# Kernel optimization log

Hardware: AMD Instinct MI355X
Metric: run time of the kernel (lower is better)

Reference implementation:

```python
import jax, jax.numpy as jnp
import numpy as np

N = 50000      # nodes
E = 400000     # edges
CIN = 15
HID = 128
HEADS = 4
NC = 2
EPS_BN = 1e-5


def _bn(x, g, b, m, v):
    # BatchNorm1d in eval mode: running stats
    return g * (x - m) * jax.lax.rsqrt(v + EPS_BN) + b


def _gat(x, src, dst, w, a_s, a_d, bias):
    # PyG GATConv(heads=4, concat=False): adds self-loops, per-head attention,
    # softmax over incoming edges (grouped by dst), mean over heads + bias.
    sl = jnp.arange(N, dtype=src.dtype)
    src = jnp.concatenate([src, sl]); dst = jnp.concatenate([dst, sl])
    h = (x @ w).reshape(N, HEADS, HID)                     # [N,H,C]
    a_src = jnp.einsum('nhc,hc->nh', h, a_s)               # [N,H]
    a_dst = jnp.einsum('nhc,hc->nh', h, a_d)
    e = jax.nn.leaky_relu(a_src[src] + a_dst[dst], 0.2)    # [E',H]
    m = jax.ops.segment_max(e, dst, num_segments=N)        # stable segment softmax
    ex = jnp.exp(e - m[dst])
    s = jax.ops.segment_sum(ex, dst, num_segments=N)
    alpha = ex / (s[dst] + 1e-16)
    out = jax.ops.segment_sum(alpha[:, :, None] * h[src], dst, num_segments=N)
    return out.mean(axis=1) + bias                         # concat=False -> head mean


def _gcn(x, src, dst, ew, w, bias):
    # PyG GCNConv with edge_weight: self-loops (weight 1), symmetric normalization.
    sl = jnp.arange(N, dtype=src.dtype)
    src_f = jnp.concatenate([src, sl]); dst_f = jnp.concatenate([dst, sl])
    ew_f = jnp.concatenate([ew, jnp.ones((N,), ew.dtype)])
    deg = jax.ops.segment_sum(ew_f, dst_f, num_segments=N)
    dinv = jnp.where(deg > 0, jax.lax.rsqrt(jnp.maximum(deg, 1e-12)), 0.0)
    norm = dinv[src_f] * ew_f * dinv[dst_f]
    h = x @ w
    return jax.ops.segment_sum(norm[:, None] * h[src_f], dst_f, num_segments=N) + bias


def setup_inputs() -> dict:
    key = jax.random.key(0)
    ks = iter(jax.random.split(key, 40))
    nrm = lambda s, sc: jax.random.normal(next(ks), s, jnp.float32) * sc
    H2 = HID // 2
    inp = {
        'x': jax.random.normal(next(ks), (N, CIN), jnp.float32),
        'edge_index': jax.random.randint(next(ks), (2, E), 0, N, jnp.int32),
        'edge_attr': jax.random.uniform(next(ks), (E, 1), jnp.float32),
        # GATConv params
        'w_gat': nrm((CIN, HEADS * HID), 0.25),
        'att_src': nrm((HEADS, HID), 0.1),
        'att_dst': nrm((HEADS, HID), 0.1),
        'b_gat': jnp.zeros((HID,), jnp.float32),
        # GCNConv params
        'w2': nrm((HID, HID), 0.09), 'b2': jnp.zeros((HID,), jnp.float32),
        'w3': nrm((HID, HID), 0.09), 'b3': jnp.zeros((HID,), jnp.float32),
        'w4': nrm((HID, HID), 0.09), 'b4': jnp.zeros((HID,), jnp.float32),
        # BatchNorm (4 layers stacked): gamma, beta, running_mean, running_var
        'bn_g': 1.0 + nrm((4, HID), 0.1),
        'bn_b': nrm((4, HID), 0.1),
        'bn_m': nrm((4, HID), 0.1),
        'bn_v': 1.0 + 0.1 * jax.random.uniform(next(ks), (4, HID), jnp.float32),
        # dense heads
        'w_shared': nrm((HID, HID), 0.09), 'b_shared': jnp.zeros((HID,), jnp.float32),
        'w_mask1': nrm((HID, H2), 0.09), 'b_mask1': jnp.zeros((H2,), jnp.float32),
        'w_mask2': nrm((H2, NC), 0.12), 'b_mask2': jnp.zeros((NC,), jnp.float32),
        'w_inst1': nrm((HID, H2), 0.09), 'b_inst1': jnp.zeros((H2,), jnp.float32),
        'w_inst2': nrm((H2, NC), 0.12), 'b_inst2': jnp.zeros((NC,), jnp.float32),
        'w_edge1': nrm((HID, H2), 0.09), 'b_edge1': jnp.zeros((H2,), jnp.float32),
        'w_edge2': nrm((H2, 1), 0.12), 'b_edge2': jnp.zeros((1,), jnp.float32),
    }
    return inp


def reference(x, edge_index, edge_attr, w_gat, att_src, att_dst, b_gat,
              w2, b2, w3, b3, w4, b4, bn_g, bn_b, bn_m, bn_v,
              w_shared, b_shared, w_mask1, b_mask1, w_mask2, b_mask2,
              w_inst1, b_inst1, w_inst2, b_inst2, w_edge1, b_edge1, w_edge2, b_edge2):
    src, dst = edge_index[0], edge_index[1]
    ew = edge_attr.squeeze(-1)
    h = jax.nn.relu(_bn(_gat(x, src, dst, w_gat, att_src, att_dst, b_gat),
                        bn_g[0], bn_b[0], bn_m[0], bn_v[0]))
    h = jax.nn.relu(_bn(_gcn(h, src, dst, ew, w2, b2), bn_g[1], bn_b[1], bn_m[1], bn_v[1]))
    h = jax.nn.relu(_bn(_gcn(h, src, dst, ew, w3, b3), bn_g[2], bn_b[2], bn_m[2], bn_v[2]))
    h = jax.nn.relu(_bn(_gcn(h, src, dst, ew, w4, b4), bn_g[3], bn_b[3], bn_m[3], bn_v[3]))
    hs = jax.nn.relu(h @ w_shared + b_shared)
    hm = jax.nn.relu(hs @ w_mask1 + b_mask1)
    mask_out = hm @ w_mask2 + b_mask2
    hi = jax.nn.relu(hs @ w_inst1 + b_inst1)
    instance_out = hi @ w_inst2 + b_inst2
    he = jax.nn.relu(hs @ w_edge1 + b_edge1)
    edge_out = he @ w_edge2 + b_edge2
    return (mask_out, instance_out, edge_out)
```

## Files before the change

kernel.cpp:

```cpp
#include <hip/hip_runtime.h>
#include <hip/hip_bf16.h>

#define NNODES 50000
#define NEDGES 400000
#define ETOT   (NEDGES + NNODES)
#define CIN    15
#define HID    128
#define HEADS  4
#define EPS_BN 1e-5f
#define NB_SCAN ((NNODES + 255) / 256)
#define NTILES  ((NNODES + 63) / 64)

typedef __attribute__((ext_vector_type(8))) short bf16x8_t;
typedef __attribute__((ext_vector_type(4))) float f32x4_t;

__device__ __forceinline__ float bfu(unsigned short u) {
  return __uint_as_float(((unsigned)u) << 16);
}
__device__ __forceinline__ unsigned short f2bf(float x) {
  union { __hip_bfloat16 b; unsigned short u; } c;
  c.b = __float2bfloat16(x);
  return c.u;
}
__device__ __forceinline__ float lrelu02(float x) {
  return x > 0.0f ? x : 0.2f * x;
}

template <int WPT, int KT, int NBLK>
__global__ __launch_bounds__(256) void gemm_mfma_kernel(
    const float* __restrict__ A, const unsigned short* __restrict__ WTh,
    const unsigned short* __restrict__ WTl, const float* __restrict__ bias,
    const float* __restrict__ bg, const float* __restrict__ bb,
    const float* __restrict__ bm, const float* __restrict__ bv,
    void* __restrict__ Cout, int act, int obf16) {
  constexpr int NC = WPT * 64;
  constexpr int CST = NC + 4;
  constexpr int CPR = KT / 8;
  constexpr int NKC = KT / 32;
  constexpr int ABYTES = 64 * KT * 2 * 2;
  constexpr int CBYTES = 64 * CST * 4;
  constexpr int SBYTES = (ABYTES > CBYTES) ? ABYTES : CBYTES;
  __shared__ __align__(16) char smem[SBYTES];
  unsigned short* Ah = (unsigned short*)smem;
  unsigned short* Al = Ah + 64 * KT;
  float* Cs = (float*)smem;

  const int tid = threadIdx.x;
  const int wv = tid >> 6, l = tid & 63;
  const int lcol = l & 15;
  const int kg = (l >> 4) << 3;
  const int colbase = wv * (WPT * 16);

  bf16x8_t hbh[NKC][WPT], hbl[NKC][WPT];
#pragma unroll
  for (int kc = 0; kc < NKC; ++kc)
#pragma unroll
    for (int jj = 0; jj < WPT; ++jj) {
      size_t boff = (size_t)(colbase + jj * 16 + lcol) * KT + kc * 32 + kg;
      hbh[kc][jj] = *(const bf16x8_t*)(WTh + boff);
      hbl[kc][jj] = *(const bf16x8_t*)(WTl + boff);
    }

  for (int tile = blockIdx.x; tile < NTILES; tile += NBLK) {
    const int bm_ = tile * 64;
    __syncthreads();

#pragma unroll
    for (int i = 0; i < (64 * CPR) / 256; ++i) {
      int cch = tid + 256 * i;
      int r = cch / CPR, k0 = (cch % CPR) << 3;
      int gr = bm_ + r;
      float v[8];
      if (gr < NNODES) {
        float4 v0 = *(const float4*)&A[(size_t)gr * KT + k0];
        float4 v1 = *(const float4*)&A[(size_t)gr * KT + k0 + 4];
        v[0] = v0.x; v[1] = v0.y; v[2] = v0.z; v[3] = v0.w;
        v[4] = v1.x; v[5] = v1.y; v[6] = v1.z; v[7] = v1.w;
      } else {
#pragma unroll
        for (int j = 0; j < 8; ++j) v[j] = 0.0f;
      }
      bf16x8_t hv, lv;
#pragma unroll
      for (int j = 0; j < 8; ++j) {
        unsigned short h = f2bf(v[j]);
        hv[j] = (short)h;
        lv[j] = (short)f2bf(v[j] - bfu(h));
      }
      int byte = (k0 << 1) ^ ((r & 7) << 4);
      *(bf16x8_t*)((char*)(Ah + r * KT) + byte) = hv;
      *(bf16x8_t*)((char*)(Al + r * KT) + byte) = lv;
    }
    __syncthreads();

    f32x4_t acc[4][WPT];
#pragma unroll
    for (int rt = 0; rt < 4; ++rt)
#pragma unroll
      for (int jj = 0; jj < WPT; ++jj) acc[rt][jj] = (f32x4_t){0.f, 0.f, 0.f, 0.f};

#pragma unroll
    for (int kc = 0; kc < NKC; ++kc) {
      int k = kc * 32 + kg;
#pragma unroll
      for (int rt = 0; rt < 4; ++rt) {
        int lrow = rt * 16 + (l & 15);
        int byte = (k << 1) ^ ((lrow & 7) << 4);
        bf16x8_t ah = *(const bf16x8_t*)((const char*)(Ah + lrow * KT) + byte);
        bf16x8_t al = *(const bf16x8_t*)((const char*)(Al + lrow * KT) + byte);
#pragma unroll
        for (int jj = 0; jj < WPT; ++jj) {
          acc[rt][jj] = __builtin_amdgcn_mfma_f32_16x16x32_bf16(ah, hbh[kc][jj], acc[rt][jj], 0, 0, 0);
          acc[rt][jj] = __builtin_amdgcn_mfma_f32_16x16x32_bf16(ah, hbl[kc][jj], acc[rt][jj], 0, 0, 0);
          acc[rt][jj] = __builtin_amdgcn_mfma_f32_16x16x32_bf16(al, hbh[kc][jj], acc[rt][jj], 0, 0, 0);
        }
      }
    }

    __syncthreads();
#pragma unroll
    for (int rt = 0; rt < 4; ++rt) {
      int trow0 = rt * 16 + ((l >> 4) << 2);
#pragma unroll
      for (int jj = 0; jj < WPT; ++jj) {
        int col = colbase + jj * 16 + lcol;
        float bs = bias ? bias[col] : 0.0f;
#pragma unroll
        for (int r = 0; r < 4; ++r) {
          float vv = acc[rt][jj][r] + bs;
          if (bg) vv = bg[col] * (vv - bm[col]) * rsqrtf(bv[col] + EPS_BN) + bb[col];
          if (act) vv = fmaxf(vv, 0.0f);
          Cs[(trow0 + r) * CST + col] = vv;
        }
      }
    }
    __syncthreads();

    constexpr int NJ = (64 * NC) / 1024;
#pragma unroll
    for (int j = 0; j < NJ; ++j) {
      int f = tid * 4 + j * 1024;
      int r = f / NC, c = f - r * NC;
      int grow = bm_ + r;
      if (grow >= NNODES) continue;
      float4 v = *(const float4*)&Cs[r * CST + c];
      if (obf16) {
        ushort4 us;
        us.x = f2bf(v.x); us.y = f2bf(v.y); us.z = f2bf(v.z); us.w = f2bf(v.w);
        *(ushort4*)&((unsigned short*)Cout)[(size_t)grow * NC + c] = us;
      } else {
        *(float4*)&((float*)Cout)[(size_t)grow * NC + c] = v;
      }
    }
  }
}

template <int NBLK>
__global__ __launch_bounds__(256) void shared_heads_kernel(
    const float* __restrict__ A, const unsigned short* __restrict__ WSh,
    const unsigned short* __restrict__ WSl, const float* __restrict__ b_shared,
    const unsigned short* __restrict__ W2h, const unsigned short* __restrict__ W2l,
    const float* __restrict__ b192,
    const float* __restrict__ w_m2, const float* __restrict__ b_m2,
    const float* __restrict__ w_i2, const float* __restrict__ b_i2,
    const float* __restrict__ w_e2, const float* __restrict__ b_e2,
    float* __restrict__ out) {
  constexpr int KT = 128;
  constexpr int CST = 196;
  constexpr int AC_BYTES = 64 * CST * 4;
  __shared__ __align__(16) char smem[AC_BYTES + 64 * KT * 2 * 2];
  unsigned short* Ah = (unsigned short*)smem;
  unsigned short* Al = Ah + 64 * KT;
  float* Cs = (float*)smem;
  unsigned short* Hh = (unsigned short*)(smem + AC_BYTES);
  unsigned short* Hl = Hh + 64 * KT;

  const int tid = threadIdx.x;
  const int wv = tid >> 6, l = tid & 63;
  const int lcol = l & 15;
  const int kg = (l >> 4) << 3;

  bf16x8_t sbh[4][2], sbl[4][2];
  {
    const int colbase = wv * 32;
#pragma unroll
    for (int kc = 0; kc < 4; ++kc)
#pragma unroll
      for (int jj = 0; jj < 2; ++jj) {
        size_t boff = (size_t)(colbase + jj * 16 + lcol) * KT + kc * 32 + kg;
        sbh[kc][jj] = *(const bf16x8_t*)(WSh + boff);
        sbl[kc][jj] = *(const bf16x8_t*)(WSl + boff);
      }
  }

  for (int tile = blockIdx.x; tile < NTILES; tile += NBLK) {
    const int bm_ = tile * 64;
    __syncthreads();

#pragma unroll
    for (int i = 0; i < 4; ++i) {
      int cch = tid + 256 * i;
      int r = cch >> 4, k0 = (cch & 15) << 3;
      int gr = bm_ + r;
      float v[8];
      if (gr < NNODES) {
        float4 v0 = *(const float4*)&A[(size_t)gr * KT + k0];
        float4 v1 = *(const float4*)&A[(size_t)gr * KT + k0 + 4];
        v[0] = v0.x; v[1] = v0.y; v[2] = v0.z; v[3] = v0.w;
        v[4] = v1.x; v[5] = v1.y; v[6] = v1.z; v[7] = v1.w;
      } else {
#pragma unroll
        for (int j = 0; j < 8; ++j) v[j] = 0.0f;
      }
      bf16x8_t hv, lv;
#pragma unroll
      for (int j = 0; j < 8; ++j) {
        unsigned short h = f2bf(v[j]);
        hv[j] = (short)h;
        lv[j] = (short)f2bf(v[j] - bfu(h));
      }
      int byte = (k0 << 1) ^ ((r & 7) << 4);
      *(bf16x8_t*)((char*)(Ah + r * KT) + byte) = hv;
      *(bf16x8_t*)((char*)(Al + r * KT) + byte) = lv;
    }
    __syncthreads();

    {
      const int colbase = wv * 32;
      f32x4_t acc[4][2];
#pragma unroll
      for (int rt = 0; rt < 4; ++rt)
#pragma unroll
        for (int jj = 0; jj < 2; ++jj) acc[rt][jj] = (f32x4_t){0.f, 0.f, 0.f, 0.f};
#pragma unroll
      for (int kc = 0; kc < 4; ++kc) {
        int k = kc * 32 + kg;
#pragma unroll
        for (int rt = 0; rt < 4; ++rt) {
          int lrow = rt * 16 + (l & 15);
          int byte = (k << 1) ^ ((lrow & 7) << 4);
          bf16x8_t ah = *(const bf16x8_t*)((const char*)(Ah + lrow * KT) + byte);
          bf16x8_t al = *(const bf16x8_t*)((const char*)(Al + lrow * KT) + byte);
#pragma unroll
          for (int jj = 0; jj < 2; ++jj) {
            acc[rt][jj] = __builtin_amdgcn_mfma_f32_16x16x32_bf16(ah, sbh[kc][jj], acc[rt][jj], 0, 0, 0);
            acc[rt][jj] = __builtin_amdgcn_mfma_f32_16x16x32_bf16(ah, sbl[kc][jj], acc[rt][jj], 0, 0, 0);
            acc[rt][jj] = __builtin_amdgcn_mfma_f32_16x16x32_bf16(al, sbh[kc][jj], acc[rt][jj], 0, 0, 0);
          }
        }
      }
#pragma unroll
      for (int rt = 0; rt < 4; ++rt) {
        int trow0 = rt * 16 + ((l >> 4) << 2);
#pragma unroll
        for (int jj = 0; jj < 2; ++jj) {
          int col = colbase + jj * 16 + lcol;
          float bs = b_shared[col];
#pragma unroll
          for (int r = 0; r < 4; ++r) {
            int trow = trow0 + r;
            float vv = fmaxf(acc[rt][jj][r] + bs, 0.0f);
            unsigned short hv = f2bf(vv);
            unsigned short lv = f2bf(vv - bfu(hv));
            int byte = ((trow * KT + col) << 1) ^ ((trow & 7) << 4);
            *(unsigned short*)((char*)Hh + byte) = hv;
            *(unsigned short*)((char*)Hl + byte) = lv;
          }
        }
      }
    }
    __syncthreads();

    {
      const int colbase = wv * 48;
      f32x4_t acc[4][3];
#pragma unroll
      for (int rt = 0; rt < 4; ++rt)
#pragma unroll
        for (int jj = 0; jj < 3; ++jj) acc[rt][jj] = (f32x4_t){0.f, 0.f, 0.f, 0.f};
#pragma unroll
      for (int kc = 0; kc < 4; ++kc) {
        bf16x8_t cbh[3], cbl[3];
#pragma unroll
        for (int jj = 0; jj < 3; ++jj) {
          size_t boff = (size_t)(colbase + jj * 16 + lcol) * KT + kc * 32 + kg;
          cbh[jj] = *(const bf16x8_t*)(W2h + boff);
          cbl[jj] = *(const bf16x8_t*)(W2l + boff);
        }
        int k = kc * 32 + kg;
#pragma unroll
        for (int rt = 0; rt < 4; ++rt) {
          int lrow = rt * 16 + (l & 15);
          int byte = (k << 1) ^ ((lrow & 7) << 4);
          bf16x8_t ah = *(const bf16x8_t*)((const char*)(Hh + lrow * KT) + byte);
          bf16x8_t al = *(const bf16x8_t*)((const char*)(Hl + lrow * KT) + byte);
#pragma unroll
          for (int jj = 0; jj < 3; ++jj) {
            acc[rt][jj] = __builtin_amdgcn_mfma_f32_16x16x32_bf16(ah, cbh[jj], acc[rt][jj], 0, 0, 0);
            acc[rt][jj] = __builtin_amdgcn_mfma_f32_16x16x32_bf16(ah, cbl[jj], acc[rt][jj], 0, 0, 0);
            acc[rt][jj] = __builtin_amdgcn_mfma_f32_16x16x32_bf16(al, cbh[jj], acc[rt][jj], 0, 0, 0);
          }
        }
      }
#pragma unroll
      for (int rt = 0; rt < 4; ++rt) {
        int trow0 = rt * 16 + ((l >> 4) << 2);
#pragma unroll
        for (int jj = 0; jj < 3; ++jj) {
          int col = colbase + jj * 16 + lcol;
          float bs = b192[col];
#pragma unroll
          for (int r = 0; r < 4; ++r) {
            float vv = fmaxf(acc[rt][jj][r] + bs, 0.0f);
            Cs[(trow0 + r) * CST + col] = vv;
          }
        }
      }
    }
    __syncthreads();

    {
      int r = tid >> 2, q = tid & 3;
      int grow = bm_ + r;
      const float* row = &Cs[r * CST];
      float p0 = 0.f, p1 = 0.f, p2 = 0.f, p3 = 0.f, p4 = 0.f;
#pragma unroll
      for (int e = 0; e < 16; ++e) {
        int c = q * 16 + e;
        float hm = row[c], hi = row[64 + c], he = row[128 + c];
        p0 += hm * w_m2[c * 2 + 0];
        p1 += hm * w_m2[c * 2 + 1];
        p2 += hi * w_i2[c * 2 + 0];
        p3 += hi * w_i2[c * 2 + 1];
        p4 += he * w_e2[c];
      }
#pragma unroll
      for (int off = 1; off < 4; off <<= 1) {
        p0 += __shfl_xor(p0, off);
        p1 += __shfl_xor(p1, off);
        p2 += __shfl_xor(p2, off);
        p3 += __shfl_xor(p3, off);
        p4 += __shfl_xor(p4, off);
      }
      if (q == 0 && grow < NNODES) {
        out[grow * 2 + 0] = p0 + b_m2[0];
        out[grow * 2 + 1] = p1 + b_m2[1];
        out[2 * NNODES + grow * 2 + 0] = p2 + b_i2[0];
        out[2 * NNODES + grow * 2 + 1] = p3 + b_i2[1];
        out[4 * NNODES + grow] = p4 + b_e2[0];
      }
    }
  }
}

__global__ void prep_att_kernel(const float* __restrict__ w,
                                const float* __restrict__ att_s,
                                const float* __restrict__ att_d,
                                float* __restrict__ wv_s,
                                float* __restrict__ wv_d) {
  int t = threadIdx.x;
  if (t >= 60) return;
  int k = t / 4, h = t & 3;
  float s = 0.f, d = 0.f;
  for (int c = 0; c < 128; ++c) {
    float wk = w[(size_t)k * 512 + h * 128 + c];
    s += wk * att_s[h * 128 + c];
    d += wk * att_d[h * 128 + c];
  }
  wv_s[k * 4 + h] = s;
  wv_d[k * 4 + h] = d;
}

__global__ void pack_wtp_kernel(const float* __restrict__ w,
                                unsigned short* __restrict__ WTh,
                                unsigned short* __restrict__ WTl) {
  int i = blockIdx.x * blockDim.x + threadIdx.x;
  if (i >= 128 * 64) return;
  int c = i >> 6, j = i & 63;
  float xv = 0.f;
  if (j < 60) {
    int h = j / 15, k = j - h * 15;
    xv = 0.25f * w[(size_t)k * 512 + h * 128 + c];
  }
  unsigned short hh = f2bf(xv);
  WTh[i] = hh;
  WTl[i] = f2bf(xv - bfu(hh));
}

__global__ __launch_bounds__(256) void a_sd_kernel(
    const float* __restrict__ x, const float* __restrict__ wv_s,
    const float* __restrict__ wv_d, float* __restrict__ a_s,
    float* __restrict__ a_d) {
  __shared__ float xs[256 * 15];
  __shared__ float wvs[60], wvd[60];
  int t = threadIdx.x;
  int base = blockIdx.x * 256;
  if (t < 60) { wvs[t] = wv_s[t]; wvd[t] = wv_d[t]; }
  for (int i = t; i < 256 * 15; i += 256) {
    int gi = base * 15 + i;
    xs[i] = (gi < NNODES * 15) ? x[gi] : 0.0f;
  }
  __syncthreads();
  int n = base + t;
  if (n >= NNODES) return;
  float a0 = 0, a1 = 0, a2 = 0, a3 = 0, d0 = 0, d1 = 0, d2 = 0, d3 = 0;
#pragma unroll
  for (int k = 0; k < 15; ++k) {
    float xv = xs[t * 15 + k];
    a0 += xv * wvs[k * 4 + 0]; a1 += xv * wvs[k * 4 + 1];
    a2 += xv * wvs[k * 4 + 2]; a3 += xv * wvs[k * 4 + 3];
    d0 += xv * wvd[k * 4 + 0]; d1 += xv * wvd[k * 4 + 1];
    d2 += xv * wvd[k * 4 + 2]; d3 += xv * wvd[k * 4 + 3];
  }
  float4 A; A.x = a0; A.y = a1; A.z = a2; A.w = a3;
  float4 D; D.x = d0; D.y = d1; D.z = d2; D.w = d3;
  *(float4*)&a_s[n * 4] = A;
  *(float4*)&a_d[n * 4] = D;
}

__global__ __launch_bounds__(256) void gat_fused_kernel(
    const float* __restrict__ x, const float* __restrict__ a_s,
    const float* __restrict__ a_d, const int* __restrict__ rowptr,
    const int* __restrict__ csr_src, float* __restrict__ g) {
  int wid = threadIdx.x >> 6, lane = threadIdx.x & 63;
  int n = blockIdx.x * 4 + wid;
  if (n >= NNODES) return;
  int e0 = rowptr[n], e1 = rowptr[n + 1];
  bool on = lane < 60;
  int h = on ? (lane / 15) : 0;
  int k = on ? (lane - h * 15) : 0;
  float adn = a_d[n * 4 + h];

  float ssum = 0.f, acc = 0.f;
  int e = e0;
  for (; e + 4 <= e1; e += 4) {
    int s0 = csr_src[e + 0], s1 = csr_src[e + 1];
    int s2 = csr_src[e + 2], s3 = csr_src[e + 3];
    float as0 = a_s[s0 * 4 + h], as1 = a_s[s1 * 4 + h];
    float as2 = a_s[s2 * 4 + h], as3 = a_s[s3 * 4 + h];
    float x0 = x[(size_t)s0 * CIN + k], x1 = x[(size_t)s1 * CIN + k];
    float x2 = x[(size_t)s2 * CIN + k], x3 = x[(size_t)s3 * CIN + k];
    float ex0 = __expf(lrelu02(as0 + adn));
    float ex1 = __expf(lrelu02(as1 + adn));
    float ex2 = __expf(lrelu02(as2 + adn));
    float ex3 = __expf(lrelu02(as3 + adn));
    ssum += (ex0 + ex1) + (ex2 + ex3);
    acc += ex0 * x0 + ex1 * x1 + ex2 * x2 + ex3 * x3;
  }
  for (; e < e1; ++e) {
    int s = csr_src[e];
    float ex = __expf(lrelu02(a_s[s * 4 + h] + adn));
    ssum += ex;
    acc += ex * x[(size_t)s * CIN + k];
  }
  g[(size_t)n * 64 + lane] = on ? acc / (ssum + 1e-16f) : 0.0f;
}

__global__ void pack_wt4_kernel(
    const float* __restrict__ w2, const float* __restrict__ w3,
    const float* __restrict__ w4, const float* __restrict__ ws,
    unsigned short* __restrict__ Hbase, unsigned short* __restrict__ Lbase) {
  int i = blockIdx.x * blockDim.x + threadIdx.x;
  if (i >= 128 * 128) return;
  const float* W = (blockIdx.y == 0) ? w2 : (blockIdx.y == 1) ? w3
                 : (blockIdx.y == 2) ? w4 : ws;
  unsigned short* Wh = Hbase + (size_t)blockIdx.y * 128 * 128;
  unsigned short* Wl = Lbase + (size_t)blockIdx.y * 128 * 128;
  int k = i >> 7, n = i & 127;
  float x = W[i];
  unsigned short h = f2bf(x);
  Wh[n * 128 + k] = h;
  Wl[n * 128 + k] = f2bf(x - bfu(h));
}

__global__ void pack_wt192_kernel(
    const float* __restrict__ w_m1, const float* __restrict__ w_i1,
    const float* __restrict__ w_e1, const float* __restrict__ b_m1,
    const float* __restrict__ b_i1, const float* __restrict__ b_e1,
    unsigned short* __restrict__ WTh, unsigned short* __restrict__ WTl,
    float* __restrict__ b192) {
  int i = blockIdx.x * blockDim.x + threadIdx.x;
  if (i < 192 * 128) {
    int n = i >> 7, k = i & 127;
    float x = (n < 64) ? w_m1[k * 64 + n]
            : (n < 128) ? w_i1[k * 64 + (n - 64)]
                        : w_e1[k * 64 + (n - 128)];
    unsigned short h = f2bf(x);
    WTh[(size_t)n * 128 + k] = h;
    WTl[(size_t)n * 128 + k] = f2bf(x - bfu(h));
  }
  if (i < 192) {
    b192[i] = (i < 64) ? b_m1[i] : (i < 128) ? b_i1[i - 64] : b_e1[i - 128];
  }
}

__global__ void count_deg_kernel(const int* __restrict__ ei,
                                 const float* __restrict__ ea,
                                 int* __restrict__ cnt,
                                 float* __restrict__ deg) {
  int i = blockIdx.x * blockDim.x + threadIdx.x;
  if (i >= ETOT) return;
  int d; float w;
  if (i < NEDGES) { d = ei[NEDGES + i]; w = ea[i]; }
  else            { d = i - NEDGES; w = 1.0f; }
  atomicAdd(&cnt[d], 1);
  atomicAdd(&deg[d], w);
}

__global__ __launch_bounds__(256) void csr_reduce_kernel(
    const int* __restrict__ cnt, int* __restrict__ bsum) {
  __shared__ int red[256];
  int t = threadIdx.x;
  int i = blockIdx.x * 256 + t;
  red[t] = (i < NNODES) ? cnt[i] : 0;
  __syncthreads();
  for (int off = 128; off > 0; off >>= 1) {
    if (t < off) red[t] += red[t + off];
    __syncthreads();
  }
  if (t == 0) bsum[blockIdx.x] = red[0];
}

__global__ __launch_bounds__(256) void csr_scanb_kernel(
    const int* __restrict__ bsum, int* __restrict__ boff) {
  __shared__ int s[256];
  int t = threadIdx.x;
  s[t] = (t < NB_SCAN) ? bsum[t] : 0;
  __syncthreads();
  for (int off = 1; off < 256; off <<= 1) {
    int u = (t >= off) ? s[t - off] : 0;
    __syncthreads();
    s[t] += u;
    __syncthreads();
  }
  if (t < NB_SCAN) boff[t] = (t == 0) ? 0 : s[t - 1];
}

__global__ __launch_bounds__(256) void csr_scan_kernel(
    int* __restrict__ cnt, const int* __restrict__ boff,
    int* __restrict__ rowptr) {
  __shared__ int s[256];
  int t = threadIdx.x;
  int i = blockIdx.x * 256 + t;
  int v = (i < NNODES) ? cnt[i] : 0;
  s[t] = v;
  __syncthreads();
  for (int off = 1; off < 256; off <<= 1) {
    int u = (t >= off) ? s[t - off] : 0;
    __syncthreads();
    s[t] += u;
    __syncthreads();
  }
  if (i < NNODES) {
    rowptr[i] = boff[blockIdx.x] + s[t] - v;
    cnt[i] = 0;
  }
  if (i == 0) rowptr[NNODES] = ETOT;
}

__global__ void dinv_kernel(const float* __restrict__ deg,
                            float* __restrict__ dinv) {
  int n = blockIdx.x * blockDim.x + threadIdx.x;
  if (n >= NNODES) return;
  float s = deg[n];
  dinv[n] = (s > 0.0f) ? rsqrtf(fmaxf(s, 1e-12f)) : 0.0f;
}

__global__ void scatter_kernel(const int* __restrict__ ei,
                               const float* __restrict__ ea,
                               const float* __restrict__ dinv,
                               const int* __restrict__ rowptr,
                               int* __restrict__ cursor,
                               int* __restrict__ csr_src,
                               float* __restrict__ csr_ew) {
  int i = blockIdx.x * blockDim.x + threadIdx.x;
  if (i >= ETOT) return;
  int s, d; float w;
  if (i < NEDGES) { s = ei[i]; d = ei[NEDGES + i]; w = ea[i]; }
  else            { s = d = i - NEDGES; w = 1.0f; }
  int pos = rowptr[d] + atomicAdd(&cursor[d], 1);
  csr_src[pos] = s;
  csr_ew[pos] = dinv[s] * w * dinv[d];
}

__global__ __launch_bounds__(256) void gcn_gather_kernel(
    const __hip_bfloat16* __restrict__ h, const int* __restrict__ rowptr,
    const int* __restrict__ csr_src, const float* __restrict__ csr_w,
    const float* __restrict__ bias,
    const float* __restrict__ bg, const float* __restrict__ bb,
    const float* __restrict__ bm, const float* __restrict__ bv,
    float* __restrict__ out) {
  int wid = threadIdx.x >> 6, lane = threadIdx.x & 63;
  int n = blockIdx.x * 4 + wid;
  if (n >= NNODES) return;
  int e0 = rowptr[n], e1 = rowptr[n + 1];
  int c = 2 * lane;
  float ax = 0.f, ay = 0.f;
  int e = e0;
  for (; e + 4 <= e1; e += 4) {
    int s0 = csr_src[e + 0], s1 = csr_src[e + 1];
    int s2 = csr_src[e + 2], s3 = csr_src[e + 3];
    float w0 = csr_w[e + 0], w1 = csr_w[e + 1];
    float w2 = csr_w[e + 2], w3 = csr_w[e + 3];
    ushort2 u0 = *(const ushort2*)(h + (size_t)s0 * HID + c);
    ushort2 u1 = *(const ushort2*)(h + (size_t)s1 * HID + c);
    ushort2 u2 = *(const ushort2*)(h + (size_t)s2 * HID + c);
    ushort2 u3 = *(const ushort2*)(h + (size_t)s3 * HID + c);
    ax += w0 * bfu(u0.x) + w1 * bfu(u1.x) + w2 * bfu(u2.x) + w3 * bfu(u3.x);
    ay += w0 * bfu(u0.y) + w1 * bfu(u1.y) + w2 * bfu(u2.y) + w3 * bfu(u3.y);
  }
  for (; e < e1; ++e) {
    int s = csr_src[e];
    float w = csr_w[e];
    ushort2 u = *(const ushort2*)(h + (size_t)s * HID + c);
    ax += w * bfu(u.x);
    ay += w * bfu(u.y);
  }
  float ox = ax + bias[c];
  float oy = ay + bias[c + 1];
  ox = bg[c] * (ox - bm[c]) * rsqrtf(bv[c] + EPS_BN) + bb[c];
  oy = bg[c + 1] * (oy - bm[c + 1]) * rsqrtf(bv[c + 1] + EPS_BN) + bb[c + 1];
  ox = fmaxf(ox, 0.0f); oy = fmaxf(oy, 0.0f);
  float2 o; o.x = ox; o.y = oy;
  *(float2*)&out[(size_t)n * HID + c] = o;
}

extern "C" void kernel_launch(void* const* d_in, const int* in_sizes, int n_in,
                              void* d_out, int out_size, void* d_ws, size_t ws_size,
                              hipStream_t stream) {
  const float* x       = (const float*)d_in[0];
  const int*   ei      = (const int*)d_in[1];
  const float* ea      = (const float*)d_in[2];
  const float* w_gat   = (const float*)d_in[3];
  const float* att_src = (const float*)d_in[4];
  const float* att_dst = (const float*)d_in[5];
  const float* b_gat   = (const float*)d_in[6];
  const float* w2 = (const float*)d_in[7];  const float* b2 = (const float*)d_in[8];
  const float* w3 = (const float*)d_in[9];  const float* b3 = (const float*)d_in[10];
  const float* w4 = (const float*)d_in[11]; const float* b4 = (const float*)d_in[12];
  const float* bn_g = (const float*)d_in[13];
  const float* bn_b = (const float*)d_in[14];
  const float* bn_m = (const float*)d_in[15];
  const float* bn_v = (const float*)d_in[16];
  const float* w_shared = (const float*)d_in[17]; const float* b_shared = (const float*)d_in[18];
  const float* w_m1 = (const float*)d_in[19]; const float* b_m1 = (const float*)d_in[20];
  const float* w_m2 = (const float*)d_in[21]; const float* b_m2 = (const float*)d_in[22];
  const float* w_i1 = (const float*)d_in[23]; const float* b_i1 = (const float*)d_in[24];
  const float* w_i2 = (const float*)d_in[25]; const float* b_i2 = (const float*)d_in[26];
  const float* w_e1 = (const float*)d_in[27]; const float* b_e1 = (const float*)d_in[28];
  const float* w_e2 = (const float*)d_in[29]; const float* b_e2 = (const float*)d_in[30];
  float* out = (float*)d_out;

  size_t off = 0;
  auto alloc = [&](size_t bytes) -> char* {
    char* p = (char*)d_ws + off;
    off += (bytes + 255) & ~(size_t)255;
    return p;
  };
  float* p0      = (float*)alloc((size_t)NNODES * HID * 4);
  float* p1      = (float*)alloc((size_t)NNODES * HID * 4);
  float* g       = (float*)alloc((size_t)NNODES * 64 * 4);
  __hip_bfloat16* hb = (__hip_bfloat16*)alloc((size_t)NNODES * HID * 2);
  float* a_s     = (float*)alloc((size_t)NNODES * 4 * 4);
  float* a_d     = (float*)alloc((size_t)NNODES * 4 * 4);
  float* deg     = (float*)alloc((size_t)NNODES * 4);
  float* dinv    = (float*)alloc((size_t)NNODES * 4);
  float* csr_ew  = (float*)alloc((size_t)ETOT * 4);
  int*   rowptr  = (int*)alloc((size_t)(NNODES + 1) * 4);
  int*   cnt     = (int*)alloc((size_t)NNODES * 4);
  int*   csr_src = (int*)alloc((size_t)ETOT * 4);
  int*   bsum    = (int*)alloc((size_t)NB_SCAN * 4);
  int*   boff    = (int*)alloc((size_t)NB_SCAN * 4);
  unsigned short* wtH = (unsigned short*)alloc(4 * 128 * 128 * 2);
  unsigned short* wtL = (unsigned short*)alloc(4 * 128 * 128 * 2);
  unsigned short* wt192h = (unsigned short*)alloc(192 * 128 * 2);
  unsigned short* wt192l = (unsigned short*)alloc(192 * 128 * 2);
  unsigned short* wtph = (unsigned short*)alloc(128 * 64 * 2);
  unsigned short* wtpl = (unsigned short*)alloc(128 * 64 * 2);
  float* b192 = (float*)alloc(192 * 4);
  float* wv_s = (float*)alloc(60 * 4);
  float* wv_d = (float*)alloc(60 * 4);

  unsigned short* wt2h = wtH + 0 * 16384; unsigned short* wt2l = wtL + 0 * 16384;
  unsigned short* wt3h = wtH + 1 * 16384; unsigned short* wt3l = wtL + 1 * 16384;
  unsigned short* wt4h = wtH + 2 * 16384; unsigned short* wt4l = wtL + 2 * 16384;
  unsigned short* wsh  = wtH + 3 * 16384; unsigned short* wsl  = wtL + 3 * 16384;

  dim3 blk256(256);
  dim3 wgrid((NNODES + 3) / 4);

  hipMemsetAsync(cnt, 0, NNODES * 4, stream);
  hipMemsetAsync(deg, 0, NNODES * 4, stream);
  count_deg_kernel<<<(ETOT + 255) / 256, blk256, 0, stream>>>(ei, ea, cnt, deg);
  csr_reduce_kernel<<<NB_SCAN, blk256, 0, stream>>>(cnt, bsum);
  csr_scanb_kernel<<<1, blk256, 0, stream>>>(bsum, boff);
  csr_scan_kernel<<<NB_SCAN, blk256, 0, stream>>>(cnt, boff, rowptr);
  dinv_kernel<<<(NNODES + 255) / 256, blk256, 0, stream>>>(deg, dinv);
  scatter_kernel<<<(ETOT + 255) / 256, blk256, 0, stream>>>(
      ei, ea, dinv, rowptr, cnt, csr_src, csr_ew);

  prep_att_kernel<<<1, 64, 0, stream>>>(w_gat, att_src, att_dst, wv_s, wv_d);
  pack_wtp_kernel<<<(128 * 64 + 255) / 256, blk256, 0, stream>>>(w_gat, wtph, wtpl);
  pack_wt4_kernel<<<dim3((128 * 128 + 255) / 256, 4), blk256, 0, stream>>>(
      w2, w3, w4, w_shared, wtH, wtL);
  pack_wt192_kernel<<<(192 * 128 + 255) / 256, blk256, 0, stream>>>(
      w_m1, w_i1, w_e1, b_m1, b_i1, b_e1, wt192h, wt192l, b192);

  a_sd_kernel<<<NB_SCAN, blk256, 0, stream>>>(x, wv_s, wv_d, a_s, a_d);

  gat_fused_kernel<<<wgrid, blk256, 0, stream>>>(
      x, a_s, a_d, rowptr, csr_src, g);

  gemm_mfma_kernel<2, 64, 512><<<512, blk256, 0, stream>>>(
      g, wtph, wtpl, b_gat, bn_g + 0, bn_b + 0, bn_m + 0, bn_v + 0, p0, 1, 0);

  gemm_mfma_kernel<2, 128, 512><<<512, blk256, 0, stream>>>(
      p0, wt2h, wt2l, nullptr, nullptr, nullptr, nullptr, nullptr, hb, 0, 1);
  gcn_gather_kernel<<<wgrid, blk256, 0, stream>>>(
      hb, rowptr, csr_src, csr_ew, b2,
      bn_g + 128, bn_b + 128, bn_m + 128, bn_v + 128, p1);

  gemm_mfma_kernel<2, 128, 512><<<512, blk256, 0, stream>>>(
      p1, wt3h, wt3l, nullptr, nullptr, nullptr, nullptr, nullptr, hb, 0, 1);
  gcn_gather_kernel<<<wgrid, blk256, 0, stream>>>(
      hb, rowptr, csr_src, csr_ew, b3,
      bn_g + 256, bn_b + 256, bn_m + 256, bn_v + 256, p0);

  gemm_mfma_kernel<2, 128, 512><<<512, blk256, 0, stream>>>(
      p0, wt4h, wt4l, nullptr, nullptr, nullptr, nullptr, nullptr, hb, 0, 1);
  gcn_gather_kernel<<<wgrid, blk256, 0, stream>>>(
      hb, rowptr, csr_src, csr_ew, b4,
      bn_g + 384, bn_b + 384, bn_m + 384, bn_v + 384, p1);

  shared_heads_kernel<196><<<196, blk256, 0, stream>>>(
      p1, wsh, wsl, b_shared, wt192h, wt192l, b192,
      w_m2, b_m2, w_i2, b_i2, w_e2, b_e2, out);
}
```

Measured before the change: 317.8 us.

## Prefetch next tile's A rows into registers during MFMA compute in GEMM kernels

Both persistent MFMA GEMM kernels now load the next tile's fp32 A rows into registers right after the LDS store barrier. The loads are issued before the current tile's MFMA loop, so global-load latency overlaps with compute instead of stalling at the start of each tile. The cost is about 32 extra VGPRs per thread for the prefetch buffer, which could lower occupancy or cause spills in kernels that already hold the weight fragments in registers.

```diff
diff --git a/kernel.cpp b/kernel.cpp
--- a/kernel.cpp
+++ b/kernel.cpp
@@ -37,6 +37,7 @@
   constexpr int CST = NC + 4;
   constexpr int CPR = KT / 8;
   constexpr int NKC = KT / 32;
+  constexpr int NIT = (64 * CPR) / 256;
   constexpr int ABYTES = 64 * KT * 2 * 2;
   constexpr int CBYTES = 64 * CST * 4;
   constexpr int SBYTES = (ABYTES > CBYTES) ? ABYTES : CBYTES;
@@ -61,37 +62,66 @@
       hbl[kc][jj] = *(const bf16x8_t*)(WTl + boff);
     }
 
-  for (int tile = blockIdx.x; tile < NTILES; tile += NBLK) {
-    const int bm_ = tile * 64;
-    __syncthreads();
-
-#pragma unroll
-    for (int i = 0; i < (64 * CPR) / 256; ++i) {
+  float pref[NIT][8];
+
+  {
+    const int bm_ = blockIdx.x * 64;
+#pragma unroll
+    for (int i = 0; i < NIT; ++i) {
       int cch = tid + 256 * i;
       int r = cch / CPR, k0 = (cch % CPR) << 3;
       int gr = bm_ + r;
-      float v[8];
       if (gr < NNODES) {
         float4 v0 = *(const float4*)&A[(size_t)gr * KT + k0];
         float4 v1 = *(const float4*)&A[(size_t)gr * KT + k0 + 4];
-        v[0] = v0.x; v[1] = v0.y; v[2] = v0.z; v[3] = v0.w;
-        v[4] = v1.x; v[5] = v1.y; v[6] = v1.z; v[7] = v1.w;
+        pref[i][0] = v0.x; pref[i][1] = v0.y; pref[i][2] = v0.z; pref[i][3] = v0.w;
+        pref[i][4] = v1.x; pref[i][5] = v1.y; pref[i][6] = v1.z; pref[i][7] = v1.w;
       } else {
 #pragma unroll
-        for (int j = 0; j < 8; ++j) v[j] = 0.0f;
-      }
+        for (int j = 0; j < 8; ++j) pref[i][j] = 0.0f;
+      }
+    }
+  }
+
+  for (int tile = blockIdx.x; tile < NTILES; tile += NBLK) {
+    const int bm_ = tile * 64;
+    __syncthreads();
+
+#pragma unroll
+    for (int i = 0; i < NIT; ++i) {
+      int cch = tid + 256 * i;
+      int r = cch / CPR, k0 = (cch % CPR) << 3;
       bf16x8_t hv, lv;
 #pragma unroll
       for (int j = 0; j < 8; ++j) {
-        unsigned short h = f2bf(v[j]);
+        unsigned short h = f2bf(pref[i][j]);
         hv[j] = (short)h;
-        lv[j] = (short)f2bf(v[j] - bfu(h));
+        lv[j] = (short)f2bf(pref[i][j] - bfu(h));
       }
       int byte = (k0 << 1) ^ ((r & 7) << 4);
       *(bf16x8_t*)((char*)(Ah + r * KT) + byte) = hv;
       *(bf16x8_t*)((char*)(Al + r * KT) + byte) = lv;
     }
     __syncthreads();
+
+    if (tile + NBLK < NTILES) {
+      const int bm2 = (tile + NBLK) * 64;
+#pragma unroll
+      for (int i = 0; i < NIT; ++i) {
+        int cch = tid + 256 * i;
+        int r = cch / CPR, k0 = (cch % CPR) << 3;
+        int gr = bm2 + r;
+        if (gr < NNODES) {
+          float4 v0 = *(const float4*)&A[(size_t)gr * KT + k0];
+          float4 v1 = *(const float4*)&A[(size_t)gr * KT + k0 + 4];
+          pref[i][0] = v0.x; pref[i][1] = v0.y; pref[i][2] = v0.z; pref[i][3] = v0.w;
+          pref[i][4] = v1.x; pref[i][5] = v1.y; pref[i][6] = v1.z; pref[i][7] = v1.w;
+        } else {
+#pragma unroll
+          for (int j = 0; j < 8; ++j) pref[i][j] = 0.0f;
+        }
+      }
+    }
 
     f32x4_t acc[4][WPT];
 #pragma unroll
@@ -193,37 +223,66 @@
       }
   }
 
-  for (int tile = blockIdx.x; tile < NTILES; tile += NBLK) {
-    const int bm_ = tile * 64;
-    __syncthreads();
-
+  float pref[4][8];
+
+  {
+    const int bm_ = blockIdx.x * 64;
 #pragma unroll
     for (int i = 0; i < 4; ++i) {
       int cch = tid + 256 * i;
       int r = cch >> 4, k0 = (cch & 15) << 3;
       int gr = bm_ + r;
-      float v[8];
       if (gr < NNODES) {
         float4 v0 = *(const float4*)&A[(size_t)gr * KT + k0];
         float4 v1 = *(const float4*)&A[(size_t)gr * KT + k0 + 4];
-        v[0] = v0.x; v[1] = v0.y; v[2] = v0.z; v[3] = v0.w;
-        v[4] = v1.x; v[5] = v1.y; v[6] = v1.z; v[7] = v1.w;
+        pref[i][0] = v0.x; pref[i][1] = v0.y; pref[i][2] = v0.z; pref[i][3] = v0.w;
+        pref[i][4] = v1.x; pref[i][5] = v1.y; pref[i][6] = v1.z; pref[i][7] = v1.w;
       } else {
 #pragma unroll
-        for (int j = 0; j < 8; ++j) v[j] = 0.0f;
-      }
+        for (int j = 0; j < 8; ++j) pref[i][j] = 0.0f;
+      }
+    }
+  }
+
+  for (int tile = blockIdx.x; tile < NTILES; tile += NBLK) {
+    const int bm_ = tile * 64;
+    __syncthreads();
+
+#pragma unroll
+    for (int i = 0; i < 4; ++i) {
+      int cch = tid + 256 * i;
+      int r = cch >> 4, k0 = (cch & 15) << 3;
       bf16x8_t hv, lv;
 #pragma unroll
       for (int j = 0; j < 8; ++j) {
-        unsigned short h = f2bf(v[j]);
+        unsigned short h = f2bf(pref[i][j]);
         hv[j] = (short)h;
-        lv[j] = (short)f2bf(v[j] - bfu(h));
+        lv[j] = (short)f2bf(pref[i][j] - bfu(h));
       }
       int byte = (k0 << 1) ^ ((r & 7) << 4);
       *(bf16x8_t*)((char*)(Ah + r * KT) + byte) = hv;
       *(bf16x8_t*)((char*)(Al + r * KT) + byte) = lv;
     }
     __syncthreads();
+
+    if (tile + NBLK < NTILES) {
+      const int bm2 = (tile + NBLK) * 64;
+#pragma unroll
+      for (int i = 0; i < 4; ++i) {
+        int cch = tid + 256 * i;
+        int r = cch >> 4, k0 = (cch & 15) << 3;
+        int gr = bm2 + r;
+        if (gr < NNODES) {
+          float4 v0 = *(const float4*)&A[(size_t)gr * KT + k0];
+          float4 v1 = *(const float4*)&A[(size_t)gr * KT + k0 + 4];
+          pref[i][0] = v0.x; pref[i][1] = v0.y; pref[i][2] = v0.z; pref[i][3] = v0.w;
+          pref[i][4] = v1.x; pref[i][5] = v1.y; pref[i][6] = v1.z; pref[i][7] = v1.w;
+        } else {
+#pragma unroll
+          for (int j = 0; j < 8; ++j) pref[i][j] = 0.0f;
+        }
+      }
+    }
 
     {
       const int colbase = wv * 32;
```

Result: no change. 317.9 us (+0.0%).
